# Kernel optimization log

Hardware: AMD Instinct MI355X
Metric: run time of the kernel (lower is better)

## Reference

```python
import jax, jax.numpy as jnp
import numpy as np

NCLASS = 21  # num_classes from init
EPS = 1e-6


def setup_inputs() -> dict:
    key = jax.random.key(0)
    k1, k2 = jax.random.split(key)
    feats = jax.random.normal(k1, (8, 256, 64, 64), dtype=jnp.float32)
    masks = jax.random.randint(k2, (8, 256, 256), 0, NCLASS, dtype=jnp.int32)
    return {"feats": feats, "masks": masks}


def reference(feats, masks):
    # feats: [B, C, h, w] float; masks: [B, H, W] int labels
    B, C, _, _ = feats.shape
    H, W = masks.shape[-2:]
    # F.interpolate(..., mode='bilinear', align_corners=False) == half-pixel bilinear resize
    f = jax.image.resize(feats, (B, C, H, W), method="bilinear")  # [B,C,H,W]
    f_flat = f.reshape(B, C, H * W)  # [B,C,P]

    # labels > nclass (e.g. 255 ignore) are clamped to the dump bucket `nclass`;
    # pixels with label == nclass are excluded (one_hot drops out-of-range rows).
    lbl = jnp.where(masks > NCLASS, NCLASS, masks).reshape(B, H * W)  # [B,P]
    onehot = jax.nn.one_hot(lbl, NCLASS, dtype=f.dtype)  # [B,P,K], dump bucket -> all zeros

    # segment-reduce: per-image per-class feature sums and pixel counts
    sums = jnp.einsum("bcp,bpk->bkc", f_flat, onehot)  # [B,K,C]
    counts = onehot.sum(axis=1)  # [B,K]
    per_img = sums / (counts[..., None] + EPS)  # [B,K,C]; absent classes -> ~0, matching torch loop skip
    prototypes = per_img.mean(axis=0)  # [K,C] (sum over batch / b)
    return prototypes
```

## Files before the change

### kernel.cpp

```cpp
#include <hip/hip_runtime.h>

#define NK 21
#define NC 256
#define NSRC 64
#define NOUT 256
#define NB 8
#define NSL 64
#define NG 8
#define EPS 1e-6f

__device__ __forceinline__ void lds_fadd(float* p, float v) {
  __hip_atomic_fetch_add(p, v, __ATOMIC_RELAXED, __HIP_MEMORY_SCOPE_WORKGROUP);
}

__device__ __forceinline__ float d4(float s, float4 a, float4 w) {
  s = fmaf(a.x, w.x, s); s = fmaf(a.y, w.y, s);
  s = fmaf(a.z, w.z, s); return fmaf(a.w, w.w, s);
}

__global__ __launch_bounds__(256, 2)
void proto_main(const float* __restrict__ feats,
                const int* __restrict__ masks,
                float* __restrict__ psum,
                float* __restrict__ pcnt) {
  __shared__ __align__(16) float Wl[NK * 64];
  __shared__ __align__(16) float Red[NK * NC];
  __shared__ int hist[NK];

  const int tid = threadIdx.x;
  const int r0 = blockIdx.x;
  const int bi = blockIdx.y;
  const int w = tid >> 6;
  const int l = tid & 63;
  const int z = w >> 1;
  const int c0 = ((w & 1) << 7) | (l << 1);

  int ylo = 4 * r0 - 2; if (ylo < 0) ylo = 0;
  int yhi = 4 * r0 + 5; if (yhi > NOUT - 1) yhi = NOUT - 1;
  const int nr = yhi - ylo + 1;
  const int x = tid;
  int lab[8];
#pragma unroll
  for (int j = 0; j < 8; ++j)
    lab[j] = (j < nr) ? masks[((size_t)bi * NOUT + ylo + j) * NOUT + x] : NK;

  const float4* fA = (const float4*)(feats + (((size_t)(bi * NC + c0)) << 12) +
                                     (size_t)r0 * 64 + 32 * z);
  const float4* fB = (const float4*)((const float*)fA + 4096);
  const float4 a0 = fA[0], a1 = fA[1], a2 = fA[2], a3 = fA[3];
  const float4 a4 = fA[4], a5 = fA[5], a6 = fA[6], a7 = fA[7];
  const float4 e0 = fB[0], e1 = fB[1], e2 = fB[2], e3 = fB[3];
  const float4 e4 = fB[4], e5 = fB[5], e6 = fB[6], e7 = fB[7];

  for (int i = tid; i < NK * 64; i += 256) Wl[i] = 0.f;
  if (tid < NK) hist[tid] = 0;
  __syncthreads();

  const int rx = x >> 2, px = x & 3;
  const int j0x = (px < 2) ? rx - 1 : rx;
  const float fx = (px == 0) ? 0.625f : (px == 1) ? 0.875f
                 : (px == 2) ? 0.125f : 0.375f;
  const int cx0 = (j0x < 0) ? 0 : j0x;
  const int cx1 = (j0x + 1 > NSRC - 1) ? NSRC - 1 : j0x + 1;
  const float wx0 = 1.f - fx, wx1 = fx;

#pragma unroll
  for (int j = 0; j < 8; ++j) {
    if (j < nr) {
      const int y = ylo + j;
      const int lbl = lab[j];
      if ((unsigned)lbl < NK) {
        const int ry = y >> 2, py = y & 3;
        const int j0y = (py < 2) ? ry - 1 : ry;
        const float fy = (py == 0) ? 0.625f : (py == 1) ? 0.875f
                       : (py == 2) ? 0.125f : 0.375f;
        const int ry0 = (j0y < 0) ? 0 : j0y;
        const int ry1 = (j0y + 1 > NSRC - 1) ? NSRC - 1 : j0y + 1;
        float* Wk = &Wl[lbl << 6];
        if (ry0 == r0) {
          lds_fadd(&Wk[cx0], (1.f - fy) * wx0);
          lds_fadd(&Wk[cx1], (1.f - fy) * wx1);
        }
        if (ry1 == r0) {
          lds_fadd(&Wk[cx0], fy * wx0);
          lds_fadd(&Wk[cx1], fy * wx1);
        }
        if ((unsigned)(y - 4 * r0) < 4u)
          atomicAdd(&hist[lbl], 1);
      }
    }
  }
  __syncthreads();

  float accA[NK], accB[NK];
#pragma unroll
  for (int k = 0; k < NK; ++k) { accA[k] = 0.f; accB[k] = 0.f; }

  const float4* wb = (const float4*)&Wl[z * 32];
#pragma unroll
  for (int k = 0; k < NK; ++k) {
    const float4 w0 = wb[k * 16 + 0], w1 = wb[k * 16 + 1];
    const float4 w2 = wb[k * 16 + 2], w3 = wb[k * 16 + 3];
    const float4 w4 = wb[k * 16 + 4], w5 = wb[k * 16 + 5];
    const float4 w6 = wb[k * 16 + 6], w7 = wb[k * 16 + 7];
    float sA = accA[k];
    sA = d4(sA, a0, w0); sA = d4(sA, a1, w1); sA = d4(sA, a2, w2); sA = d4(sA, a3, w3);
    sA = d4(sA, a4, w4); sA = d4(sA, a5, w5); sA = d4(sA, a6, w6); sA = d4(sA, a7, w7);
    accA[k] = sA;
    float sB = accB[k];
    sB = d4(sB, e0, w0); sB = d4(sB, e1, w1); sB = d4(sB, e2, w2); sB = d4(sB, e3, w3);
    sB = d4(sB, e4, w4); sB = d4(sB, e5, w5); sB = d4(sB, e6, w6); sB = d4(sB, e7, w7);
    accB[k] = sB;
  }

  if (w >= 2) {
#pragma unroll
    for (int k = 0; k < NK; ++k)
      *(float2*)&Red[k * NC + c0] = make_float2(accA[k], accB[k]);
  }
  __syncthreads();
  if (w < 2) {
    float* dst = psum + ((size_t)(bi * NSL + r0) * NK) * NC + c0;
#pragma unroll
    for (int k = 0; k < NK; ++k) {
      const float2 r = *(const float2*)&Red[k * NC + c0];
      *(float2*)&dst[k * NC] = make_float2(accA[k] + r.x, accB[k] + r.y);
    }
  }
  if (tid < NK) pcnt[(size_t)(bi * NSL + r0) * NK + tid] = (float)hist[tid];
}

__global__ __launch_bounds__(256)
void proto_finalA(const float* __restrict__ psum,
                  const float* __restrict__ pcnt,
                  float* __restrict__ psum2,
                  float* __restrict__ pcnt2) {
  const int k = blockIdx.x;
  const int b = blockIdx.y;
  const int g = blockIdx.z;
  const int c = threadIdx.x;
  const int sl0 = g * (NSL / NG);
  float s = 0.f, cnt = 0.f;
#pragma unroll
  for (int j = 0; j < NSL / NG; ++j) {
    s += psum[((size_t)(b * NSL + sl0 + j) * NK + k) * NC + c];
    cnt += pcnt[(size_t)(b * NSL + sl0 + j) * NK + k];
  }
  psum2[((size_t)(b * NG + g) * NK + k) * NC + c] = s;
  if (c == 0) pcnt2[(size_t)(b * NG + g) * NK + k] = cnt;
}

__global__ __launch_bounds__(256)
void proto_finalB(const float* __restrict__ psum2,
                  const float* __restrict__ pcnt2,
                  float* __restrict__ out) {
  const int k = blockIdx.x;
  const int c = threadIdx.x;
  float a = 0.f;
#pragma unroll
  for (int b = 0; b < NB; ++b) {
    float s = 0.f, cnt = 0.f;
#pragma unroll
    for (int g = 0; g < NG; ++g) {
      s += psum2[((size_t)(b * NG + g) * NK + k) * NC + c];
      cnt += pcnt2[(size_t)(b * NG + g) * NK + k];
    }
    a += s / (cnt + EPS);
  }
  out[(size_t)k * NC + c] = a * 0.125f;
}

extern "C" void kernel_launch(void* const* d_in, const int* in_sizes, int n_in,
                              void* d_out, int out_size, void* d_ws, size_t ws_size,
                              hipStream_t stream) {
  const float* feats = (const float*)d_in[0];
  const int* masks = (const int*)d_in[1];
  float* out = (float*)d_out;

  float* psum = (float*)d_ws;
  float* pcnt = psum + (size_t)NB * NSL * NK * NC;
  float* psum2 = pcnt + (size_t)NB * NSL * NK;
  float* pcnt2 = psum2 + (size_t)NB * NG * NK * NC;

  proto_main<<<dim3(64, NB), 256, 0, stream>>>(feats, masks, psum, pcnt);
  proto_finalA<<<dim3(NK, NB, NG), 256, 0, stream>>>(psum, pcnt, psum2, pcnt2);
  proto_finalB<<<dim3(NK), 256, 0, stream>>>(psum2, pcnt2, out);
}
```

Before: 100.5 us.

## Fuse reduction kernels into main via global atomics and last-block finalize

Replaces the two follow-up reduction kernels with float atomic adds into four striped per-image accumulators plus a last-block-done counter. The final block computes the per-class mean and writes the output. This removes two kernel launches and the round trip of partial sums through memory. In exchange it adds a memset, atomic contention, and a serial finalize done by a single block.

```diff
diff --git a/kernel.cpp b/kernel.cpp
--- a/kernel.cpp
+++ b/kernel.cpp
@@ -5,8 +5,8 @@
 #define NSRC 64
 #define NOUT 256
 #define NB 8
-#define NSL 64
-#define NG 8
+#define NS 4
+#define NBLK (64 * NB)
 #define EPS 1e-6f
 
 __device__ __forceinline__ void lds_fadd(float* p, float v) {
@@ -19,13 +19,16 @@
 }
 
 __global__ __launch_bounds__(256, 2)
-void proto_main(const float* __restrict__ feats,
-                const int* __restrict__ masks,
-                float* __restrict__ psum,
-                float* __restrict__ pcnt) {
+void proto_fused(const float* __restrict__ feats,
+                 const int* __restrict__ masks,
+                 float* __restrict__ accum,
+                 float* __restrict__ cnt,
+                 int* __restrict__ done,
+                 float* __restrict__ out) {
   __shared__ __align__(16) float Wl[NK * 64];
   __shared__ __align__(16) float Red[NK * NC];
   __shared__ int hist[NK];
+  __shared__ int lastFlag;
 
   const int tid = threadIdx.x;
   const int r0 = blockIdx.x;
@@ -119,55 +122,45 @@
       *(float2*)&Red[k * NC + c0] = make_float2(accA[k], accB[k]);
   }
   __syncthreads();
+
   if (w < 2) {
-    float* dst = psum + ((size_t)(bi * NSL + r0) * NK) * NC + c0;
+    float* dst = accum + ((size_t)((r0 & (NS - 1)) * NB + bi) * NK) * NC + c0;
 #pragma unroll
     for (int k = 0; k < NK; ++k) {
       const float2 r = *(const float2*)&Red[k * NC + c0];
-      *(float2*)&dst[k * NC] = make_float2(accA[k] + r.x, accB[k] + r.y);
+      atomicAdd(&dst[k * NC + 0], accA[k] + r.x);
+      atomicAdd(&dst[k * NC + 1], accB[k] + r.y);
     }
   }
-  if (tid < NK) pcnt[(size_t)(bi * NSL + r0) * NK + tid] = (float)hist[tid];
-}
+  if (tid < NK) atomicAdd(&cnt[bi * NK + tid], (float)hist[tid]);
 
-__global__ __launch_bounds__(256)
-void proto_finalA(const float* __restrict__ psum,
-                  const float* __restrict__ pcnt,
-                  float* __restrict__ psum2,
-                  float* __restrict__ pcnt2) {
-  const int k = blockIdx.x;
-  const int b = blockIdx.y;
-  const int g = blockIdx.z;
-  const int c = threadIdx.x;
-  const int sl0 = g * (NSL / NG);
-  float s = 0.f, cnt = 0.f;
+  if (tid == 0) {
+    __threadfence();
+    const int d = __hip_atomic_fetch_add(done, 1, __ATOMIC_ACQ_REL,
+                                         __HIP_MEMORY_SCOPE_AGENT);
+    lastFlag = (d == NBLK - 1);
+  }
+  __syncthreads();
+  if (!lastFlag) return;
+
+  const int c = tid;
 #pragma unroll
-  for (int j = 0; j < NSL / NG; ++j) {
-    s += psum[((size_t)(b * NSL + sl0 + j) * NK + k) * NC + c];
-    cnt += pcnt[(size_t)(b * NSL + sl0 + j) * NK + k];
+  for (int k = 0; k < NK; ++k) {
+    float a = 0.f;
+#pragma unroll
+    for (int b = 0; b < NB; ++b) {
+      float s = 0.f;
+#pragma unroll
+      for (int s2 = 0; s2 < NS; ++s2)
+        s += __hip_atomic_load(
+            &accum[((size_t)(s2 * NB + b) * NK + k) * NC + c],
+            __ATOMIC_RELAXED, __HIP_MEMORY_SCOPE_AGENT);
+      const float ct = __hip_atomic_load(&cnt[b * NK + k], __ATOMIC_RELAXED,
+                                         __HIP_MEMORY_SCOPE_AGENT);
+      a += s / (ct + EPS);
+    }
+    out[(size_t)k * NC + c] = a * 0.125f;
   }
-  psum2[((size_t)(b * NG + g) * NK + k) * NC + c] = s;
-  if (c == 0) pcnt2[(size_t)(b * NG + g) * NK + k] = cnt;
-}
-
-__global__ __launch_bounds__(256)
-void proto_finalB(const float* __restrict__ psum2,
-                  const float* __restrict__ pcnt2,
-                  float* __restrict__ out) {
-  const int k = blockIdx.x;
-  const int c = threadIdx.x;
-  float a = 0.f;
-#pragma unroll
-  for (int b = 0; b < NB; ++b) {
-    float s = 0.f, cnt = 0.f;
-#pragma unroll
-    for (int g = 0; g < NG; ++g) {
-      s += psum2[((size_t)(b * NG + g) * NK + k) * NC + c];
-      cnt += pcnt2[(size_t)(b * NG + g) * NK + k];
-    }
-    a += s / (cnt + EPS);
-  }
-  out[(size_t)k * NC + c] = a * 0.125f;
 }
 
 extern "C" void kernel_launch(void* const* d_in, const int* in_sizes, int n_in,
@@ -177,12 +170,12 @@
   const int* masks = (const int*)d_in[1];
   float* out = (float*)d_out;
 
-  float* psum = (float*)d_ws;
-  float* pcnt = psum + (size_t)NB * NSL * NK * NC;
-  float* psum2 = pcnt + (size_t)NB * NSL * NK;
-  float* pcnt2 = psum2 + (size_t)NB * NG * NK * NC;
+  float* accum = (float*)d_ws;
+  float* cnt = accum + (size_t)NS * NB * NK * NC;
+  int* done = (int*)(cnt + (size_t)NB * NK);
+  const size_t zero_bytes =
+      ((size_t)NS * NB * NK * NC + (size_t)NB * NK) * sizeof(float) + sizeof(int);
 
-  proto_main<<<dim3(64, NB), 256, 0, stream>>>(feats, masks, psum, pcnt);
-  proto_finalA<<<dim3(NK, NB, NG), 256, 0, stream>>>(psum, pcnt, psum2, pcnt2);
-  proto_finalB<<<dim3(NK), 256, 0, stream>>>(psum2, pcnt2, out);
+  hipMemsetAsync(d_ws, 0, zero_bytes, stream);
+  proto_fused<<<dim3(64, NB), 256, 0, stream>>>(feats, masks, accum, cnt, done, out);
 }
```

After: 138.9 us. +38.2%, slower.

## Fuse final reduction kernels via last-block counter and split classes across waves

Applied to the files above, without the earlier changes.

The two finalize kernels are merged into one. A per-class atomic done counter lets the last arriving block do the cross-batch mean, which removes one kernel launch. The main kernel's work is remapped so each thread handles 4 channels and half of the classes, loading 4 channel rows of features instead of 2. Each weight LDS read is then reused across four channels, at the cost of more feature registers. The counter is reset inside proto_main, which relies on stream ordering between the kernels.

```diff
diff --git a/kernel.cpp b/kernel.cpp
--- a/kernel.cpp
+++ b/kernel.cpp
@@ -18,11 +18,42 @@
   s = fmaf(a.z, w.z, s); return fmaf(a.w, w.w, s);
 }
 
+#define KLOOP(K0, K1)                                    \
+  _Pragma("unroll")                                      \
+  for (int k = (K0); k < (K1); ++k) {                    \
+    const float4* wk = wb + k * 16;                      \
+    float4 a = acc[k - (K0)];                            \
+    _Pragma("unroll")                                    \
+    for (int s = 0; s < 8; ++s) {                        \
+      const float4 wv = wk[s];                           \
+      a.x = d4(a.x, F[0][s], wv);                        \
+      a.y = d4(a.y, F[1][s], wv);                        \
+      a.z = d4(a.z, F[2][s], wv);                        \
+      a.w = d4(a.w, F[3][s], wv);                        \
+    }                                                    \
+    acc[k - (K0)] = a;                                   \
+  }
+
+#define STORE_RED(K0, K1)                                \
+  _Pragma("unroll")                                      \
+  for (int k = (K0); k < (K1); ++k)                      \
+    *(float4*)&Red[k * NC + c0] = acc[k - (K0)];
+
+#define STORE_PSUM(K0, K1)                               \
+  _Pragma("unroll")                                      \
+  for (int k = (K0); k < (K1); ++k) {                    \
+    const float4 r = *(const float4*)&Red[k * NC + c0];  \
+    float4 a = acc[k - (K0)];                            \
+    a.x += r.x; a.y += r.y; a.z += r.z; a.w += r.w;      \
+    *(float4*)&dst[k * NC + c0] = a;                     \
+  }
+
 __global__ __launch_bounds__(256, 2)
 void proto_main(const float* __restrict__ feats,
                 const int* __restrict__ masks,
                 float* __restrict__ psum,
-                float* __restrict__ pcnt) {
+                float* __restrict__ pcnt,
+                int* __restrict__ done) {
   __shared__ __align__(16) float Wl[NK * 64];
   __shared__ __align__(16) float Red[NK * NC];
   __shared__ int hist[NK];
@@ -32,8 +63,11 @@
   const int bi = blockIdx.y;
   const int w = tid >> 6;
   const int l = tid & 63;
-  const int z = w >> 1;
-  const int c0 = ((w & 1) << 7) | (l << 1);
+  const int z = w & 1;
+  const int kh = w >> 1;
+  const int c0 = l << 2;
+
+  if (r0 == 0 && bi == 0 && tid < NK) done[tid] = 0;
 
   int ylo = 4 * r0 - 2; if (ylo < 0) ylo = 0;
   int yhi = 4 * r0 + 5; if (yhi > NOUT - 1) yhi = NOUT - 1;
@@ -44,13 +78,15 @@
   for (int j = 0; j < 8; ++j)
     lab[j] = (j < nr) ? masks[((size_t)bi * NOUT + ylo + j) * NOUT + x] : NK;
 
-  const float4* fA = (const float4*)(feats + (((size_t)(bi * NC + c0)) << 12) +
-                                     (size_t)r0 * 64 + 32 * z);
-  const float4* fB = (const float4*)((const float*)fA + 4096);
-  const float4 a0 = fA[0], a1 = fA[1], a2 = fA[2], a3 = fA[3];
-  const float4 a4 = fA[4], a5 = fA[5], a6 = fA[6], a7 = fA[7];
-  const float4 e0 = fB[0], e1 = fB[1], e2 = fB[2], e3 = fB[3];
-  const float4 e4 = fB[4], e5 = fB[5], e6 = fB[6], e7 = fB[7];
+  const float* fb = feats + (((size_t)(bi * NC + c0)) << 12) +
+                    (size_t)r0 * 64 + 32 * z;
+  float4 F[4][8];
+#pragma unroll
+  for (int ch = 0; ch < 4; ++ch) {
+    const float4* fp = (const float4*)(fb + ((size_t)ch << 12));
+#pragma unroll
+    for (int s = 0; s < 8; ++s) F[ch][s] = fp[s];
+  }
 
   for (int i = tid; i < NK * 64; i += 256) Wl[i] = 0.f;
   if (tid < NK) hist[tid] = 0;
@@ -92,80 +128,73 @@
   }
   __syncthreads();
 
-  float accA[NK], accB[NK];
-#pragma unroll
-  for (int k = 0; k < NK; ++k) { accA[k] = 0.f; accB[k] = 0.f; }
+  float4 acc[11];
+#pragma unroll
+  for (int k = 0; k < 11; ++k) acc[k] = make_float4(0.f, 0.f, 0.f, 0.f);
 
   const float4* wb = (const float4*)&Wl[z * 32];
-#pragma unroll
-  for (int k = 0; k < NK; ++k) {
-    const float4 w0 = wb[k * 16 + 0], w1 = wb[k * 16 + 1];
-    const float4 w2 = wb[k * 16 + 2], w3 = wb[k * 16 + 3];
-    const float4 w4 = wb[k * 16 + 4], w5 = wb[k * 16 + 5];
-    const float4 w6 = wb[k * 16 + 6], w7 = wb[k * 16 + 7];
-    float sA = accA[k];
-    sA = d4(sA, a0, w0); sA = d4(sA, a1, w1); sA = d4(sA, a2, w2); sA = d4(sA, a3, w3);
-    sA = d4(sA, a4, w4); sA = d4(sA, a5, w5); sA = d4(sA, a6, w6); sA = d4(sA, a7, w7);
-    accA[k] = sA;
-    float sB = accB[k];
-    sB = d4(sB, e0, w0); sB = d4(sB, e1, w1); sB = d4(sB, e2, w2); sB = d4(sB, e3, w3);
-    sB = d4(sB, e4, w4); sB = d4(sB, e5, w5); sB = d4(sB, e6, w6); sB = d4(sB, e7, w7);
-    accB[k] = sB;
-  }
-
-  if (w >= 2) {
-#pragma unroll
-    for (int k = 0; k < NK; ++k)
-      *(float2*)&Red[k * NC + c0] = make_float2(accA[k], accB[k]);
-  }
-  __syncthreads();
-  if (w < 2) {
-    float* dst = psum + ((size_t)(bi * NSL + r0) * NK) * NC + c0;
-#pragma unroll
-    for (int k = 0; k < NK; ++k) {
-      const float2 r = *(const float2*)&Red[k * NC + c0];
-      *(float2*)&dst[k * NC] = make_float2(accA[k] + r.x, accB[k] + r.y);
-    }
+  if (kh == 0) { KLOOP(0, 11) } else { KLOOP(11, 21) }
+
+  if (z == 1) {
+    if (kh == 0) { STORE_RED(0, 11) } else { STORE_RED(11, 21) }
+  }
+  __syncthreads();
+  if (z == 0) {
+    float* dst = psum + ((size_t)(bi * NSL + r0) * NK) * NC;
+    if (kh == 0) { STORE_PSUM(0, 11) } else { STORE_PSUM(11, 21) }
   }
   if (tid < NK) pcnt[(size_t)(bi * NSL + r0) * NK + tid] = (float)hist[tid];
 }
 
 __global__ __launch_bounds__(256)
-void proto_finalA(const float* __restrict__ psum,
-                  const float* __restrict__ pcnt,
-                  float* __restrict__ psum2,
-                  float* __restrict__ pcnt2) {
+void proto_final(const float* __restrict__ psum,
+                 const float* __restrict__ pcnt,
+                 float* __restrict__ psum2,
+                 float* __restrict__ pcnt2,
+                 int* __restrict__ done,
+                 float* __restrict__ out) {
+  __shared__ int lastFlag;
   const int k = blockIdx.x;
   const int b = blockIdx.y;
   const int g = blockIdx.z;
   const int c = threadIdx.x;
   const int sl0 = g * (NSL / NG);
+
   float s = 0.f, cnt = 0.f;
 #pragma unroll
   for (int j = 0; j < NSL / NG; ++j) {
     s += psum[((size_t)(b * NSL + sl0 + j) * NK + k) * NC + c];
     cnt += pcnt[(size_t)(b * NSL + sl0 + j) * NK + k];
   }
-  psum2[((size_t)(b * NG + g) * NK + k) * NC + c] = s;
-  if (c == 0) pcnt2[(size_t)(b * NG + g) * NK + k] = cnt;
-}
-
-__global__ __launch_bounds__(256)
-void proto_finalB(const float* __restrict__ psum2,
-                  const float* __restrict__ pcnt2,
-                  float* __restrict__ out) {
-  const int k = blockIdx.x;
-  const int c = threadIdx.x;
+  __hip_atomic_store(&psum2[((size_t)(b * NG + g) * NK + k) * NC + c], s,
+                     __ATOMIC_RELAXED, __HIP_MEMORY_SCOPE_AGENT);
+  if (c == 0)
+    __hip_atomic_store(&pcnt2[(size_t)(b * NG + g) * NK + k], cnt,
+                       __ATOMIC_RELAXED, __HIP_MEMORY_SCOPE_AGENT);
+
+  __syncthreads();
+  if (c == 0) {
+    __threadfence();
+    const int d = __hip_atomic_fetch_add(&done[k], 1, __ATOMIC_ACQ_REL,
+                                         __HIP_MEMORY_SCOPE_AGENT);
+    lastFlag = (d == NB * NG - 1);
+  }
+  __syncthreads();
+  if (!lastFlag) return;
+
   float a = 0.f;
 #pragma unroll
-  for (int b = 0; b < NB; ++b) {
-    float s = 0.f, cnt = 0.f;
-#pragma unroll
-    for (int g = 0; g < NG; ++g) {
-      s += psum2[((size_t)(b * NG + g) * NK + k) * NC + c];
-      cnt += pcnt2[(size_t)(b * NG + g) * NK + k];
+  for (int b2 = 0; b2 < NB; ++b2) {
+    float ss = 0.f, cc = 0.f;
+#pragma unroll
+    for (int g2 = 0; g2 < NG; ++g2) {
+      ss += __hip_atomic_load(
+          &psum2[((size_t)(b2 * NG + g2) * NK + k) * NC + c],
+          __ATOMIC_RELAXED, __HIP_MEMORY_SCOPE_AGENT);
+      cc += __hip_atomic_load(&pcnt2[(size_t)(b2 * NG + g2) * NK + k],
+                              __ATOMIC_RELAXED, __HIP_MEMORY_SCOPE_AGENT);
     }
-    a += s / (cnt + EPS);
+    a += ss / (cc + EPS);
   }
   out[(size_t)k * NC + c] = a * 0.125f;
 }
@@ -181,8 +210,9 @@
   float* pcnt = psum + (size_t)NB * NSL * NK * NC;
   float* psum2 = pcnt + (size_t)NB * NSL * NK;
   float* pcnt2 = psum2 + (size_t)NB * NG * NK * NC;
-
-  proto_main<<<dim3(64, NB), 256, 0, stream>>>(feats, masks, psum, pcnt);
-  proto_finalA<<<dim3(NK, NB, NG), 256, 0, stream>>>(psum, pcnt, psum2, pcnt2);
-  proto_finalB<<<dim3(NK), 256, 0, stream>>>(psum2, pcnt2, out);
-}
+  int* done = (int*)(pcnt2 + (size_t)NB * NG * NK);
+
+  proto_main<<<dim3(64, NB), 256, 0, stream>>>(feats, masks, psum, pcnt, done);
+  proto_final<<<dim3(NK, NB, NG), 256, 0, stream>>>(psum, pcnt, psum2, pcnt2,
+                                                    done, out);
+}
```

Measured after the change: 141.0 us. 40.4% more time.
